# Performance work log

Hardware: AMD Instinct MI355X
Metric: run time of the kernel (lower is better)

The kernel has to match this reference:

```python
import jax, jax.numpy as jnp
import numpy as np

B, L, H, F, E = 32, 512, 768, 3072, 8  # sentences, seq_len, hidden, ffn, experts


def setup_inputs() -> dict:
    key = jax.random.key(0)
    kx, kl, k1, k2, k3, k4 = jax.random.split(key, 6)
    return {
        "hidden_states": jax.random.normal(kx, (B, L, H), dtype=jnp.float32),
        "router_labels": jax.random.randint(kl, (B,), 0, E, dtype=jnp.int32),
        "W1": jax.random.normal(k1, (E, H, F), dtype=jnp.float32) * 0.02,
        "b1": jnp.zeros((E, F), dtype=jnp.float32),
        "W2": jax.random.normal(k2, (E, F, H), dtype=jnp.float32) * 0.02,
        "b2": jnp.zeros((E, H), dtype=jnp.float32),
    }


def reference(hidden_states, router_labels, W1, b1, W2, b2):
    # Equivalent to: sort sentences by label, run each group through its
    # expert FFN, concat, unsort. Expressed as a gather of per-sentence
    # expert weights followed by batched GEMMs (same math, no data-dependent
    # shapes).
    W1g = W1[router_labels]            # [B, H, F]
    b1g = b1[router_labels][:, None]   # [B, 1, F]
    W2g = W2[router_labels]            # [B, F, H]
    b2g = b2[router_labels][:, None]   # [B, 1, H]
    h = jnp.einsum("blh,bhf->blf", hidden_states, W1g) + b1g
    h = jax.nn.gelu(h, approximate=False)
    out = jnp.einsum("blf,bfh->blh", h, W2g) + b2g
    return out
```

## Files before the change

### kernel.cpp

```cpp
#include <hip/hip_runtime.h>
#include <hip/hip_bf16.h>

#define NB   32
#define SEQ  512
#define HID  768
#define FFN  3072
#define NEXP 8

typedef float f32x4 __attribute__((ext_vector_type(4)));
typedef short s16x8 __attribute__((ext_vector_type(8)));

__device__ __forceinline__ unsigned short f2bf(float f) {
    return __builtin_bit_cast(unsigned short, (__bf16)f);
}

#define GLOAD16(gp, lp) __builtin_amdgcn_global_load_lds( \
    (const __attribute__((address_space(1))) unsigned int*)(gp), \
    (__attribute__((address_space(3))) unsigned int*)(lp), 16, 0, 0)

__global__ __launch_bounds__(256) void cvt_x_kernel(
    const float* __restrict__ X, unsigned short* __restrict__ Xb, int n8)
{
    int idx = blockIdx.x * blockDim.x + threadIdx.x;
    int stride = gridDim.x * blockDim.x;
    for (int i = idx; i < n8; i += stride) {
        f32x4 a = *(const f32x4*)(X + (size_t)i * 8);
        f32x4 b = *(const f32x4*)(X + (size_t)i * 8 + 4);
        unsigned short o[8];
#pragma unroll
        for (int v = 0; v < 4; v++) o[v] = f2bf(a[v]);
#pragma unroll
        for (int v = 0; v < 4; v++) o[4 + v] = f2bf(b[v]);
        *(s16x8*)(Xb + (size_t)i * 8) = *(s16x8*)o;
    }
}

__global__ __launch_bounds__(256) void cvt_transpose_kernel(
    const float* __restrict__ W, unsigned short* __restrict__ WT, int R, int C)
{
    __shared__ unsigned short tile[64][65];
    const int cb = blockIdx.x * 64, rb = blockIdx.y * 64;
    const float* src = W + (size_t)blockIdx.z * R * C;
    unsigned short* dst = WT + (size_t)blockIdx.z * R * C;
    const int x = threadIdx.x & 63, y0 = threadIdx.x >> 6;
#pragma unroll
    for (int i = 0; i < 16; i++) {
        int r = y0 + i * 4;
        tile[r][x] = f2bf(src[(size_t)(rb + r) * C + cb + x]);
    }
    __syncthreads();
#pragma unroll
    for (int i = 0; i < 16; i++) {
        int c = y0 + i * 4;
        dst[(size_t)(cb + c) * R + rb + x] = tile[x][c];
    }
}

template<int LDB, bool ISA>
__device__ __forceinline__ void stage_region(const char* g, char* lds, int half, int tid)
{
#pragma unroll
    for (int p = 0; p < 2; p++) {
        int L  = p * 8192 + tid * 16;
        int rr = L >> 7;
        int cb = L & 127;
        int row = ISA ? ((rr & 63) + ((rr >> 6) << 7) + half * 64)
                      : ((rr & 31) + ((rr >> 5) << 6) + half * 32);
        int cbs = cb ^ ((row & 7) << 4);
        GLOAD16(g + (size_t)row * LDB + cbs, lds + (size_t)row * 128 + cb);
    }
}

template<int IH, int JH, int VM, class STG>
__device__ __forceinline__ void gphase(const char* Ab, const char* Bb,
    int arow_b, int brow_b, int k0, f32x4 (&acc)[8][4], STG&& stg)
{
    s16x8 a[2][4], b[2][2];
    const int k1 = k0 ^ 64;
#pragma unroll
    for (int i = 0; i < 4; i++) {
        const char* p = Ab + arow_b + (IH * 64 + i * 16) * 128;
        a[0][i] = *(const s16x8*)(p + k0);
        a[1][i] = *(const s16x8*)(p + k1);
    }
#pragma unroll
    for (int j = 0; j < 2; j++) {
        const char* p = Bb + brow_b + (JH * 32 + j * 16) * 128;
        b[0][j] = *(const s16x8*)(p + k0);
        b[1][j] = *(const s16x8*)(p + k1);
    }
    stg();
    __builtin_amdgcn_s_barrier();
    __builtin_amdgcn_s_setprio(1);
#pragma unroll
    for (int kk = 0; kk < 2; kk++)
#pragma unroll
        for (int i = 0; i < 4; i++)
#pragma unroll
            for (int j = 0; j < 2; j++)
                acc[IH * 4 + i][JH * 2 + j] = __builtin_amdgcn_mfma_f32_16x16x32_bf16(
                    a[kk][i], b[kk][j], acc[IH * 4 + i][JH * 2 + j], 0, 0, 0);
    __builtin_amdgcn_s_setprio(0);
    if constexpr (VM >= 0)
        asm volatile("s_waitcnt vmcnt(%0)" :: "i"(VM) : "memory");
    __builtin_amdgcn_s_barrier();
}

template<int LDB, bool S1, bool S2, int VM>
__device__ __forceinline__ void gwindow(const char* AgK, const char* BgK,
    char* Acur, char* Bcur, char* Anxt, char* Bnxt,
    int arow_b, int brow_b, int k0, int tid, f32x4 (&acc)[8][4])
{
    gphase<0, 0, -1>(Acur, Bcur, arow_b, brow_b, k0, acc,
        [&] { if constexpr (S1) stage_region<LDB, true >(AgK + 128, Anxt, 1, tid); });
    gphase<0, 1, -1>(Acur, Bcur, arow_b, brow_b, k0, acc,
        [&] { if constexpr (S1) stage_region<LDB, false>(BgK + 128, Bnxt, 1, tid); });
    gphase<1, 0, -1>(Acur, Bcur, arow_b, brow_b, k0, acc,
        [&] { if constexpr (S2) stage_region<LDB, true >(AgK + 256, Acur, 0, tid); });
    gphase<1, 1, VM>(Acur, Bcur, arow_b, brow_b, k0, acc,
        [&] { if constexpr (S2) stage_region<LDB, false>(BgK + 256, Bcur, 0, tid); });
}

template<int LDB>
__device__ __forceinline__ void gemm_mainloop(const char* Ag, const char* Bg,
    char* smem, int KT, int tid, int arow_b, int brow_b, int k0, f32x4 (&acc)[8][4])
{
    stage_region<LDB, true >(Ag,       smem,          0, tid);
    stage_region<LDB, false>(Bg,       smem + 65536,  0, tid);
    stage_region<LDB, true >(Ag,       smem,          1, tid);
    stage_region<LDB, false>(Bg,       smem + 65536,  1, tid);
    stage_region<LDB, true >(Ag + 128, smem + 32768,  0, tid);
    stage_region<LDB, false>(Bg + 128, smem + 98304,  0, tid);
    asm volatile("s_waitcnt vmcnt(4)" ::: "memory");
    __builtin_amdgcn_s_barrier();

    int cur = 0;
    for (int kt = 0; kt < KT - 2; ++kt) {
        char* Acur = smem + (cur << 15);
        char* Anxt = smem + ((cur ^ 1) << 15);
        char* Bcur = smem + 65536 + (cur << 15);
        char* Bnxt = smem + 65536 + ((cur ^ 1) << 15);
        gwindow<LDB, true, true, 4>(Ag + (size_t)kt * 128, Bg + (size_t)kt * 128,
            Acur, Bcur, Anxt, Bnxt, arow_b, brow_b, k0, tid, acc);
        cur ^= 1;
    }
    {
        char* Acur = smem + (cur << 15);
        char* Anxt = smem + ((cur ^ 1) << 15);
        char* Bcur = smem + 65536 + (cur << 15);
        char* Bnxt = smem + 65536 + ((cur ^ 1) << 15);
        gwindow<LDB, true, false, 0>(Ag + (size_t)(KT - 2) * 128, Bg + (size_t)(KT - 2) * 128,
            Acur, Bcur, Anxt, Bnxt, arow_b, brow_b, k0, tid, acc);
        cur ^= 1;
    }
    {
        char* Acur = smem + (cur << 15);
        char* Anxt = smem + ((cur ^ 1) << 15);
        char* Bcur = smem + 65536 + (cur << 15);
        char* Bnxt = smem + 65536 + ((cur ^ 1) << 15);
        gwindow<LDB, false, false, -1>(Ag + (size_t)(KT - 1) * 128, Bg + (size_t)(KT - 1) * 128,
            Acur, Bcur, Anxt, Bnxt, arow_b, brow_b, k0, tid, acc);
    }
}

__global__ __launch_bounds__(512, 2) void moe_gemm1(
    const unsigned short* __restrict__ Xb,
    const int*   __restrict__ labels,
    const unsigned short* __restrict__ W1T,
    const float* __restrict__ B1,
    unsigned short* __restrict__ G)
{
    extern __shared__ char smem[];
    const int nt = blockIdx.x, mt = blockIdx.y, bs = blockIdx.z;
    const int e  = labels[bs];

    const char* Ag = (const char*)(Xb + ((size_t)bs * SEQ + (size_t)mt * 256) * HID);
    const char* Bg = (const char*)(W1T + (size_t)e * FFN * HID + (size_t)nt * 256 * HID);

    const int tid = threadIdx.x;
    const int lane = tid & 63, w = tid >> 6;
    const int wm = (w >> 2) * 128, wn = (w & 3) * 64;
    const int fr = lane & 15, fq = lane >> 4;
    const int arow_b = (wm + fr) * 128, brow_b = (wn + fr) * 128;
    const int k0 = (fq * 16) ^ ((fr & 7) << 4);

    f32x4 acc[8][4];
#pragma unroll
    for (int i = 0; i < 8; i++)
#pragma unroll
        for (int j = 0; j < 4; j++) acc[i][j] = (f32x4)0.0f;

    gemm_mainloop<HID * 2>(Ag, Bg, smem, HID / 64, tid, arow_b, brow_b, k0, acc);

    const float* b1g = B1 + (size_t)e * FFN + (size_t)nt * 256;
    unsigned short* Cg = G + ((size_t)bs * SEQ + (size_t)mt * 256) * FFN + (size_t)nt * 256;
#pragma unroll
    for (int mi = 0; mi < 8; mi++)
#pragma unroll
        for (int nj = 0; nj < 4; nj++) {
            const int col = wn + nj * 16 + fr;
            const float bias = b1g[col];
#pragma unroll
            for (int r = 0; r < 4; r++) {
                const int row = wm + mi * 16 + fq * 4 + r;
                float v = acc[mi][nj][r] + bias;
                float g = 0.5f * v * (1.0f + erff(v * 0.70710678118654752f));
                Cg[(size_t)row * FFN + col] = f2bf(g);
            }
        }
}

__global__ __launch_bounds__(512, 2) void moe_gemm2(
    const unsigned short* __restrict__ G,
    const int*   __restrict__ labels,
    const unsigned short* __restrict__ W2T,
    const float* __restrict__ B2,
    float* __restrict__ Out)
{
    extern __shared__ char smem[];
    const int nt = blockIdx.x, mt = blockIdx.y, bs = blockIdx.z;
    const int e  = labels[bs];

    const char* Ag = (const char*)(G + ((size_t)bs * SEQ + (size_t)mt * 256) * FFN);
    const char* Bg = (const char*)(W2T + (size_t)e * HID * FFN + (size_t)nt * 256 * FFN);

    const int tid = threadIdx.x;
    const int lane = tid & 63, w = tid >> 6;
    const int wm = (w >> 2) * 128, wn = (w & 3) * 64;
    const int fr = lane & 15, fq = lane >> 4;
    const int arow_b = (wm + fr) * 128, brow_b = (wn + fr) * 128;
    const int k0 = (fq * 16) ^ ((fr & 7) << 4);

    f32x4 acc[8][4];
#pragma unroll
    for (int i = 0; i < 8; i++)
#pragma unroll
        for (int j = 0; j < 4; j++) acc[i][j] = (f32x4)0.0f;

    gemm_mainloop<FFN * 2>(Ag, Bg, smem, FFN / 64, tid, arow_b, brow_b, k0, acc);

    const float* b2g = B2 + (size_t)e * HID + (size_t)nt * 256;
    float* Cg = Out + ((size_t)bs * SEQ + (size_t)mt * 256) * HID + (size_t)nt * 256;
#pragma unroll
    for (int mi = 0; mi < 8; mi++)
#pragma unroll
        for (int nj = 0; nj < 4; nj++) {
            const int col = wn + nj * 16 + fr;
            const float bias = b2g[col];
#pragma unroll
            for (int r = 0; r < 4; r++) {
                const int row = wm + mi * 16 + fq * 4 + r;
                Cg[(size_t)row * HID + col] = acc[mi][nj][r] + bias;
            }
        }
}

extern "C" void kernel_launch(void* const* d_in, const int* in_sizes, int n_in,
                              void* d_out, int out_size, void* d_ws, size_t ws_size,
                              hipStream_t stream) {
    const float* X      = (const float*)d_in[0];
    const int*   labels = (const int*)  d_in[1];
    const float* W1     = (const float*)d_in[2];
    const float* B1     = (const float*)d_in[3];
    const float* W2     = (const float*)d_in[4];
    const float* B2     = (const float*)d_in[5];
    float* Out = (float*)d_out;

    char* ws = (char*)d_ws;
    unsigned short* Xb  = (unsigned short*)(ws);
    unsigned short* W1T = (unsigned short*)(ws + 25165824);
    unsigned short* W2T = (unsigned short*)(ws + 62914560);
    unsigned short* G   = (unsigned short*)(ws + 100663296);

    (void)hipFuncSetAttribute((const void*)moe_gemm1,
        hipFuncAttributeMaxDynamicSharedMemorySize, 131072);
    (void)hipFuncSetAttribute((const void*)moe_gemm2,
        hipFuncAttributeMaxDynamicSharedMemorySize, 131072);

    cvt_x_kernel<<<2048, 256, 0, stream>>>(X, Xb, NB * SEQ * HID / 8);
    cvt_transpose_kernel<<<dim3(FFN / 64, HID / 64, NEXP), 256, 0, stream>>>(W1, W1T, HID, FFN);
    cvt_transpose_kernel<<<dim3(HID / 64, FFN / 64, NEXP), 256, 0, stream>>>(W2, W2T, FFN, HID);

    dim3 g1(FFN / 256, SEQ / 256, NB);
    moe_gemm1<<<g1, dim3(512), 131072, stream>>>(Xb, labels, W1T, B1, G);

    dim3 g2(HID / 256, SEQ / 256, NB);
    moe_gemm2<<<g2, dim3(512), 131072, stream>>>(G, labels, W2T, B2, Out);
}
```

Baseline: 275.4 us.

## Reuse LDS fragments across MFMA quadrants and use tanh-approx GELU

The four-phase k-window is reordered (quadrants 00,01,11,10) so A and B fragments read from LDS are kept in registers and reused across phases, cutting LDS reads per window. The reads for each phase are issued before the staging and barrier rather than in a separate gphase routine. The exact erf GELU in the first GEMM epilogue is replaced with a tanh approximation built on hardware exp2/rcp, and bias loads are hoisted out of the epilogue loop. This changes numerics slightly (tanh-GELU versus exact erf) and raises register pressure from holding two B fragment sets.

```diff
diff --git a/kernel.cpp b/kernel.cpp
--- a/kernel.cpp
+++ b/kernel.cpp
@@ -12,6 +12,20 @@
 
 __device__ __forceinline__ unsigned short f2bf(float f) {
     return __builtin_bit_cast(unsigned short, (__bf16)f);
+}
+
+__device__ __forceinline__ float fast_exp2(float x) {
+    float r; asm("v_exp_f32 %0, %1" : "=v"(r) : "v"(x)); return r;
+}
+__device__ __forceinline__ float fast_rcp(float x) {
+    float r; asm("v_rcp_f32 %0, %1" : "=v"(r) : "v"(x)); return r;
+}
+
+__device__ __forceinline__ float gelu_fast(float v) {
+    float u  = v * (0.7978845608f + 0.0356774081f * v * v);
+    float t  = fast_exp2(-2.8853900817779268f * fabsf(u));
+    float T  = (1.0f - t) * fast_rcp(1.0f + t);
+    return 0.5f * v + 0.5f * fabsf(v) * T;
 }
 
 #define GLOAD16(gp, lp) __builtin_amdgcn_global_load_lds( \
@@ -71,26 +85,30 @@
     }
 }
 
-template<int IH, int JH, int VM, class STG>
-__device__ __forceinline__ void gphase(const char* Ab, const char* Bb,
-    int arow_b, int brow_b, int k0, f32x4 (&acc)[8][4], STG&& stg)
-{
-    s16x8 a[2][4], b[2][2];
+__device__ __forceinline__ void read_af(const char* Ab, int arow_b, int k0, int ih, s16x8 (&a)[2][4])
+{
     const int k1 = k0 ^ 64;
 #pragma unroll
     for (int i = 0; i < 4; i++) {
-        const char* p = Ab + arow_b + (IH * 64 + i * 16) * 128;
+        const char* p = Ab + arow_b + (ih * 64 + i * 16) * 128;
         a[0][i] = *(const s16x8*)(p + k0);
         a[1][i] = *(const s16x8*)(p + k1);
     }
+}
+__device__ __forceinline__ void read_bf(const char* Bb, int brow_b, int k0, int jh, s16x8 (&b)[2][2])
+{
+    const int k1 = k0 ^ 64;
 #pragma unroll
     for (int j = 0; j < 2; j++) {
-        const char* p = Bb + brow_b + (JH * 32 + j * 16) * 128;
+        const char* p = Bb + brow_b + (jh * 32 + j * 16) * 128;
         b[0][j] = *(const s16x8*)(p + k0);
         b[1][j] = *(const s16x8*)(p + k1);
     }
-    stg();
-    __builtin_amdgcn_s_barrier();
+}
+
+template<int IH, int JH>
+__device__ __forceinline__ void mfma_quad(s16x8 (&a)[2][4], s16x8 (&b)[2][2], f32x4 (&acc)[8][4])
+{
     __builtin_amdgcn_s_setprio(1);
 #pragma unroll
     for (int kk = 0; kk < 2; kk++)
@@ -101,9 +119,6 @@
                 acc[IH * 4 + i][JH * 2 + j] = __builtin_amdgcn_mfma_f32_16x16x32_bf16(
                     a[kk][i], b[kk][j], acc[IH * 4 + i][JH * 2 + j], 0, 0, 0);
     __builtin_amdgcn_s_setprio(0);
-    if constexpr (VM >= 0)
-        asm volatile("s_waitcnt vmcnt(%0)" :: "i"(VM) : "memory");
-    __builtin_amdgcn_s_barrier();
 }
 
 template<int LDB, bool S1, bool S2, int VM>
@@ -111,14 +126,29 @@
     char* Acur, char* Bcur, char* Anxt, char* Bnxt,
     int arow_b, int brow_b, int k0, int tid, f32x4 (&acc)[8][4])
 {
-    gphase<0, 0, -1>(Acur, Bcur, arow_b, brow_b, k0, acc,
-        [&] { if constexpr (S1) stage_region<LDB, true >(AgK + 128, Anxt, 1, tid); });
-    gphase<0, 1, -1>(Acur, Bcur, arow_b, brow_b, k0, acc,
-        [&] { if constexpr (S1) stage_region<LDB, false>(BgK + 128, Bnxt, 1, tid); });
-    gphase<1, 0, -1>(Acur, Bcur, arow_b, brow_b, k0, acc,
-        [&] { if constexpr (S2) stage_region<LDB, true >(AgK + 256, Acur, 0, tid); });
-    gphase<1, 1, VM>(Acur, Bcur, arow_b, brow_b, k0, acc,
-        [&] { if constexpr (S2) stage_region<LDB, false>(BgK + 256, Bcur, 0, tid); });
+    s16x8 a[2][4], b0[2][2], b1[2][2];
+    read_af(Acur, arow_b, k0, 0, a);
+    read_bf(Bcur, brow_b, k0, 0, b0);
+    if constexpr (S1) stage_region<LDB, true >(AgK + 128, Anxt, 1, tid);
+    __builtin_amdgcn_s_barrier();
+    mfma_quad<0, 0>(a, b0, acc);
+    __builtin_amdgcn_s_barrier();
+    read_bf(Bcur, brow_b, k0, 1, b1);
+    if constexpr (S1) stage_region<LDB, false>(BgK + 128, Bnxt, 1, tid);
+    __builtin_amdgcn_s_barrier();
+    mfma_quad<0, 1>(a, b1, acc);
+    __builtin_amdgcn_s_barrier();
+    read_af(Acur, arow_b, k0, 1, a);
+    if constexpr (S2) stage_region<LDB, true >(AgK + 256, Acur, 0, tid);
+    __builtin_amdgcn_s_barrier();
+    mfma_quad<1, 1>(a, b1, acc);
+    __builtin_amdgcn_s_barrier();
+    if constexpr (S2) stage_region<LDB, false>(BgK + 256, Bcur, 0, tid);
+    __builtin_amdgcn_s_barrier();
+    mfma_quad<1, 0>(a, b0, acc);
+    if constexpr (VM >= 0)
+        asm volatile("s_waitcnt vmcnt(%0)" :: "i"(VM) : "memory");
+    __builtin_amdgcn_s_barrier();
 }
 
 template<int LDB>
@@ -194,18 +224,19 @@
 
     const float* b1g = B1 + (size_t)e * FFN + (size_t)nt * 256;
     unsigned short* Cg = G + ((size_t)bs * SEQ + (size_t)mt * 256) * FFN + (size_t)nt * 256;
+    float bias[4];
+#pragma unroll
+    for (int nj = 0; nj < 4; nj++) bias[nj] = b1g[wn + nj * 16 + fr];
 #pragma unroll
     for (int mi = 0; mi < 8; mi++)
 #pragma unroll
         for (int nj = 0; nj < 4; nj++) {
             const int col = wn + nj * 16 + fr;
-            const float bias = b1g[col];
 #pragma unroll
             for (int r = 0; r < 4; r++) {
                 const int row = wm + mi * 16 + fq * 4 + r;
-                float v = acc[mi][nj][r] + bias;
-                float g = 0.5f * v * (1.0f + erff(v * 0.70710678118654752f));
-                Cg[(size_t)row * FFN + col] = f2bf(g);
+                float v = acc[mi][nj][r] + bias[nj];
+                Cg[(size_t)row * FFN + col] = f2bf(gelu_fast(v));
             }
         }
 }
@@ -241,16 +272,18 @@
 
     const float* b2g = B2 + (size_t)e * HID + (size_t)nt * 256;
     float* Cg = Out + ((size_t)bs * SEQ + (size_t)mt * 256) * HID + (size_t)nt * 256;
+    float bias[4];
+#pragma unroll
+    for (int nj = 0; nj < 4; nj++) bias[nj] = b2g[wn + nj * 16 + fr];
 #pragma unroll
     for (int mi = 0; mi < 8; mi++)
 #pragma unroll
         for (int nj = 0; nj < 4; nj++) {
             const int col = wn + nj * 16 + fr;
-            const float bias = b2g[col];
 #pragma unroll
             for (int r = 0; r < 4; r++) {
                 const int row = wm + mi * 16 + fq * 4 + r;
-                Cg[(size_t)row * HID + col] = acc[mi][nj][r] + bias;
+                Cg[(size_t)row * HID + col] = acc[mi][nj][r] + bias[nj];
             }
         }
 }
```

New measurement: 239.3 us. -13.1%, faster.
